# Kernel optimization log

Measured on AMD Instinct MI355X. Metric: run time of the kernel, lower is better.

The kernel has to match this reference:

```python
import jax, jax.numpy as jnp
import numpy as np

V, E, H = 1024, 32, 64
D = 8                     # number of tree levels (root at depth 0)
PER = 149796              # nodes per non-root level
N = 1 + 7 * PER           # 1048573 total nodes


def setup_inputs() -> dict:
    rng = np.random.default_rng(0)
    sizes = [1] + [PER] * (D - 1)
    off = np.concatenate([[0], np.cumsum(sizes)])
    depth = np.repeat(np.arange(D), sizes).astype(np.int64)
    parent = np.zeros(N, dtype=np.int64)  # root points to itself (harmless: its h is 0 when read)
    for l in range(1, D):
        parent[off[l]:off[l + 1]] = rng.integers(off[l - 1], off[l], sizes[l])
    token_ids = rng.integers(0, V, N).astype(np.int64)

    key = jax.random.key(0)
    ks = jax.random.split(key, 7)
    s = 0.05
    return {
        "token_ids": jnp.asarray(token_ids),
        "parent": jnp.asarray(parent),
        "depth": jnp.asarray(depth),
        "max_depth": D - 1,
        "emb": jax.random.normal(ks[0], (V, E), jnp.float32) * s,
        "W_iou_w": jax.random.normal(ks[1], (3 * H, E), jnp.float32) * s,
        "W_iou_b": jax.random.normal(ks[2], (3 * H,), jnp.float32) * s,
        "U_iou_w": jax.random.normal(ks[3], (3 * H, H), jnp.float32) * s,
        "W_f_w": jax.random.normal(ks[4], (H, E), jnp.float32) * s,
        "W_f_b": jax.random.normal(ks[5], (H,), jnp.float32) * s,
        "U_f_w": jax.random.normal(ks[6], (H, H), jnp.float32) * s,
    }


def reference(token_ids, parent, depth, max_depth, emb,
              W_iou_w, W_iou_b, U_iou_w, W_f_w, W_f_b, U_f_w):
    n = token_ids.shape[0]
    hid = U_f_w.shape[0]
    x = emb[token_ids]                                 # [N, E]
    wiou_x = x @ W_iou_w.T + W_iou_b                   # [N, 3H] (input part, precomputed)
    wf_x = x @ W_f_w.T + W_f_b                         # [N, H]
    h = jnp.zeros((n, hid), x.dtype)
    c = jnp.zeros((n, hid), x.dtype)
    # level-synchronous bottom-up sweep (deepest level first); children of a
    # depth-d node are exactly at depth d+1, already finalized when d is processed
    for d in range(max_depth, -1, -1):
        h_sum = jax.ops.segment_sum(h, parent, num_segments=n)        # child-sum per parent
        f = jax.nn.sigmoid(wf_x[parent] + h @ U_f_w.T)                # forget gate per child edge
        fc = jax.ops.segment_sum(f * c, parent, num_segments=n)      # sum_k f_k * c_k per parent
        iou = wiou_x + h_sum @ U_iou_w.T
        i, o, u = jnp.split(iou, 3, axis=-1)
        c_new = jax.nn.sigmoid(i) * jnp.tanh(u) + fc
        h_new = jax.nn.sigmoid(o) * jnp.tanh(c_new)
        m = (depth == d)[:, None]
        h = jnp.where(m, h_new, h)
        c = jnp.where(m, c_new, c)
    return h[0]  # root hidden state, matching TreeLSTMEncoder.forward
```

## Files before the change

### kernel.cpp

```cpp
#include <hip/hip_runtime.h>
#include <hip/hip_fp16.h>
#include <string.h>

#define PER  149796
#define NN   1048573
#define HDIM 64
#define EDIM 32
#define NIOU 192
#define NS   256

typedef _Float16 f16;
typedef _Float16 f16x8 __attribute__((ext_vector_type(8)));
typedef _Float16 f16x2 __attribute__((ext_vector_type(2)));
typedef float    f32x4 __attribute__((ext_vector_type(4)));

__device__ __forceinline__ float sigf(float x){ return 1.0f/(1.0f+__expf(-x)); }
__device__ __forceinline__ float tanh_f(float x){
  float ax = fabsf(x);
  float e  = __expf(-2.0f*ax);
  float t  = (1.0f - e)/(1.0f + e);
  return x < 0.0f ? -t : t;
}

__device__ __forceinline__ void atomAddH2(f16x2* p, f16 a, f16 b){
#if defined(__HIP_DEVICE_COMPILE__)
  typedef _Float16 h2 __attribute__((ext_vector_type(2)));
  h2 v; v[0]=a; v[1]=b;
  (void)__builtin_amdgcn_global_atomic_fadd_v2f16(
      (__attribute__((address_space(1))) h2*)p, v);
#else
  (void)p; (void)a; (void)b;
#endif
}

__global__ __launch_bounds__(256) void tablepack_kernel(
    const float* __restrict__ emb, const float* __restrict__ Wiou, const float* __restrict__ biou,
    const float* __restrict__ Wf, const float* __restrict__ bf,
    const float* __restrict__ Uf, const float* __restrict__ Uiou,
    float* __restrict__ embWiou, float* __restrict__ embWf,
    f16* __restrict__ Bfp, f16* __restrict__ Biop)
{
  if (blockIdx.x < 1024){
    int v = blockIdx.x;
    int m = threadIdx.x;
    const float* x = emb + (size_t)v*EDIM;
    if (m < NIOU){
      float a = biou[m];
      #pragma unroll
      for (int e=0;e<EDIM;e++) a += Wiou[m*EDIM+e]*x[e];
      embWiou[(size_t)v*NIOU + m] = a;
    } else {
      int mm = m - NIOU;
      float a = bf[mm];
      #pragma unroll
      for (int e=0;e<EDIM;e++) a += Wf[mm*EDIM+e]*x[e];
      embWf[(size_t)v*HDIM + mm] = a;
    }
  } else {
    for (int i = threadIdx.x; i < 2*4*64*8; i += 256){
      int j = i & 7, L = (i>>3)&63, st = i>>9;
      int t = st & 3, s = st >> 2;
      int k = s*32 + (L>>4)*8 + j;
      int n = t*16 + (L&15);
      Bfp[i] = (f16)Uf[n*HDIM + k];
    }
    for (int i = threadIdx.x; i < 2*12*64*8; i += 256){
      int j = i & 7, L = (i>>3)&63, st = i>>9;
      int t = st % 12, s = st / 12;
      int k = s*32 + (L>>4)*8 + j;
      int n = t*16 + (L&15);
      Biop[i] = (f16)Uiou[n*HDIM + k];
    }
  }
}

__global__ __launch_bounds__(64,4) void level_kernel(
    const int* __restrict__ tok, const int* __restrict__ parent,
    const float* __restrict__ embWiou, const float* __restrict__ embWf,
    const f16* __restrict__ Biopack, const f16* __restrict__ Ufpack,
    const f16x2* __restrict__ accIn, f16x2* __restrict__ accOut,
    float* __restrict__ rootslice,
    int poff, int ppoff, int mode)
{
  __shared__ f16 Ah[16*72];
  __shared__ f16 FAf[16*68];
  int lane = threadIdx.x;
  int j0   = blockIdx.x*16;
  int q = lane>>4, c16 = lane&15;

  const f16x8* Bp = (const f16x8*)Biopack;
  const f16x8* Up = (const f16x8*)Ufpack;

  f32x4 acc[12];
  #pragma unroll
  for (int nt=0;nt<12;nt++) acc[nt] = (f32x4){0.f,0.f,0.f,0.f};

  if (mode != 0){
    #pragma unroll
    for (int i=0;i<16;i++){
      int j = j0 + i; if (j > PER-1) j = PER-1;
      f16x2 v = accIn[(size_t)j*HDIM + lane];
      Ah[i*72 + lane]  = v.x;
      FAf[i*68 + lane] = v.y;
    }
    __syncthreads();
    f16x8 A0 = *(const f16x8*)(Ah + c16*72 + q*8);
    f16x8 A1 = *(const f16x8*)(Ah + c16*72 + 32 + q*8);
    #pragma unroll
    for (int nt=0;nt<12;nt++){
      f16x8 B0 = Bp[nt*64 + lane];
      f16x8 B1 = Bp[(12+nt)*64 + lane];
      acc[nt] = __builtin_amdgcn_mfma_f32_16x16x32_f16(A0, B0, acc[nt], 0,0,0);
      acc[nt] = __builtin_amdgcn_mfma_f32_16x16x32_f16(A1, B1, acc[nt], 0,0,0);
    }
  }

  int tok0 = (mode == 2) ? tok[0] : 0;
  float cc[4][4];
  f16   hh[4][4];
  int   prow_[4]; int wt_[4]; bool ok_[4];
  #pragma unroll
  for (int r=0;r<4;r++){
    int j = j0 + q*4 + r;
    bool ok = j < PER;
    int jl = ok ? j : PER-1;
    int g = poff + jl;
    int tk = tok[g];
    const float* tr = embWiou + (size_t)tk*NIOU;
    ok_[r] = ok;
    if (mode != 2){
      int pg = parent[g];
      prow_[r] = pg - ppoff;
      wt_[r]   = tok[pg];
    } else {
      prow_[r] = 0;
      wt_[r]   = tok0;
    }
    int lrow = q*4 + r;
    #pragma unroll
    for (int nt=0;nt<4;nt++){
      int col = nt*16 + c16;
      float ai = acc[nt][r]   + tr[col];
      float ao = acc[nt+4][r] + tr[64+col];
      float au = acc[nt+8][r] + tr[128+col];
      float fav = (mode != 0) ? (float)FAf[lrow*68 + col] : 0.0f;
      float c = sigf(ai)*tanh_f(au) + fav;
      float h = sigf(ao)*tanh_f(c);
      cc[r][nt] = c;
      hh[r][nt] = (f16)h;
    }
  }
  __syncthreads();
  #pragma unroll
  for (int r=0;r<4;r++)
    #pragma unroll
    for (int nt=0;nt<4;nt++)
      Ah[(q*4+r)*72 + nt*16 + c16] = hh[r][nt];
  __syncthreads();
  f16x8 H0 = *(const f16x8*)(Ah + c16*72 + q*8);
  f16x8 H1 = *(const f16x8*)(Ah + c16*72 + 32 + q*8);
  f32x4 g4[4];
  #pragma unroll
  for (int nt=0;nt<4;nt++) g4[nt] = (f32x4){0.f,0.f,0.f,0.f};
  #pragma unroll
  for (int nt=0;nt<4;nt++){
    f16x8 B0 = Up[nt*64 + lane];
    f16x8 B1 = Up[(4+nt)*64 + lane];
    g4[nt] = __builtin_amdgcn_mfma_f32_16x16x32_f16(H0, B0, g4[nt], 0,0,0);
    g4[nt] = __builtin_amdgcn_mfma_f32_16x16x32_f16(H1, B1, g4[nt], 0,0,0);
  }
  if (mode != 2){
    #pragma unroll
    for (int r=0;r<4;r++){
      if (!ok_[r]) continue;
      const float* wr = embWf + (size_t)wt_[r]*HDIM;
      size_t rb = (size_t)prow_[r]*HDIM;
      #pragma unroll
      for (int nt=0;nt<4;nt++){
        int col = nt*16 + c16;
        float v = sigf(g4[nt][r] + wr[col]) * cc[r][nt];
        atomAddH2(&accOut[rb + col], hh[r][nt], (f16)v);
      }
    }
  } else {
    const float* wr = embWf + (size_t)tok0*HDIM;
    float sH[4] = {0.f,0.f,0.f,0.f};
    float sF[4] = {0.f,0.f,0.f,0.f};
    #pragma unroll
    for (int r=0;r<4;r++){
      if (!ok_[r]) continue;
      #pragma unroll
      for (int nt=0;nt<4;nt++){
        int col = nt*16 + c16;
        float v = sigf(g4[nt][r] + wr[col]) * cc[r][nt];
        sH[nt] += (float)hh[r][nt];
        sF[nt] += v;
      }
    }
    int sl = blockIdx.x & (NS-1);
    #pragma unroll
    for (int nt=0;nt<4;nt++){
      int col = nt*16 + c16;
      atomicAdd(&rootslice[sl*128 + col],      sF[nt]);
      atomicAdd(&rootslice[sl*128 + 64 + col], sH[nt]);
    }
  }
}

__global__ void rootnode_kernel(
    const int* __restrict__ tok, const float* __restrict__ emb,
    const float* __restrict__ Wiou, const float* __restrict__ biou, const float* __restrict__ Uiou,
    const float* __restrict__ rootslice, float* __restrict__ out)
{
  __shared__ float hsh[64];
  int m = threadIdx.x;
  if (m >= HDIM) return;
  float fcs = 0.f, hs = 0.f;
  for (int s=0; s<NS; ++s){
    fcs += rootslice[s*128 + m];
    hs  += rootslice[s*128 + 64 + m];
  }
  hsh[m] = hs;
  __syncthreads();
  int t = tok[0];
  float ai=biou[m], ao=biou[HDIM+m], au=biou[2*HDIM+m];
  for (int e=0;e<EDIM;e++){
    float xe = emb[(size_t)t*EDIM+e];
    ai += Wiou[(size_t)m*EDIM+e]*xe;
    ao += Wiou[(size_t)(HDIM+m)*EDIM+e]*xe;
    au += Wiou[(size_t)(2*HDIM+m)*EDIM+e]*xe;
  }
  for (int k=0;k<HDIM;k++){
    float hv = hsh[k];
    ai += Uiou[(size_t)m*HDIM+k]*hv;
    ao += Uiou[(size_t)(HDIM+m)*HDIM+k]*hv;
    au += Uiou[(size_t)(2*HDIM+m)*HDIM+k]*hv;
  }
  float c = sigf(ai)*tanh_f(au) + fcs;
  out[m] = sigf(ao)*tanh_f(c);
}

static inline char* alignup(char* p){
  uintptr_t u = (uintptr_t)p;
  u = (u + 255) & ~(uintptr_t)255;
  return (char*)u;
}

extern "C" void kernel_launch(void* const* d_in, const int* in_sizes, int n_in,
                              void* d_out, int out_size, void* d_ws, size_t ws_size,
                              hipStream_t stream)
{
  const int*   tok    = (const int*)d_in[0];
  const int*   parent = (const int*)d_in[1];
  const float* emb    = (const float*)d_in[4];
  const float* Wiou   = (const float*)d_in[5];
  const float* biou   = (const float*)d_in[6];
  const float* Uiou   = (const float*)d_in[7];
  const float* Wf     = (const float*)d_in[8];
  const float* bf     = (const float*)d_in[9];
  const float* Uf     = (const float*)d_in[10];
  float* out = (float*)d_out;

  char* w = (char*)d_ws;
  size_t BUF = (size_t)PER*HDIM*sizeof(f16x2);
  f16x2* bufA      = (f16x2*)w;  w = alignup(w + BUF);
  f16x2* bufB      = (f16x2*)w;  w = alignup(w + BUF);
  float* embWiou   = (float*)w;  w = alignup(w + 1024*NIOU*sizeof(float));
  float* embWf     = (float*)w;  w = alignup(w + 1024*HDIM*sizeof(float));
  float* rootslice = (float*)w;  w = alignup(w + (size_t)NS*128*sizeof(float));
  f16*   Ufpack    = (f16*)w;    w = alignup(w + 2*4*64*8*sizeof(f16));
  f16*   Biopack   = (f16*)w;    w = alignup(w + 2*12*64*8*sizeof(f16));

  const int NB = (PER + 15)/16;

  (void)hipMemsetAsync(rootslice, 0, (size_t)NS*128*sizeof(float), stream);
  tablepack_kernel<<<1025, 256, 0, stream>>>(emb, Wiou, biou, Wf, bf, Uf, Uiou,
                                             embWiou, embWf, Ufpack, Biopack);

  (void)hipMemsetAsync(bufA, 0, BUF, stream);
  level_kernel<<<NB, 64, 0, stream>>>(tok, parent, embWiou, embWf, Biopack, Ufpack,
                                      bufB , bufA, rootslice,
                                      1 + 6*PER, 1 + 5*PER, 0);
  f16x2* accIn = bufA; f16x2* accOut = bufB;
  for (int d=6; d>=2; --d){
    (void)hipMemsetAsync(accOut, 0, BUF, stream);
    level_kernel<<<NB, 64, 0, stream>>>(tok, parent, embWiou, embWf, Biopack, Ufpack,
                                        accIn, accOut, rootslice,
                                        1 + (d-1)*PER, 1 + (d-2)*PER, 1);
    f16x2* t2 = accIn; accIn = accOut; accOut = t2;
  }
  level_kernel<<<NB, 64, 0, stream>>>(tok, parent, embWiou, embWf, Biopack, Ufpack,
                                      accIn, accOut , rootslice,
                                      1, 0, 2);

  rootnode_kernel<<<1, 64, 0, stream>>>(tok, emb, Wiou, biou, Uiou, rootslice, out);
}
```

Measured before the change: 593.5 us.

## Replace child-to-parent atomics with per-level sorted CSR segmented gather

```diff
diff --git a/kernel.cpp b/kernel.cpp
--- a/kernel.cpp
+++ b/kernel.cpp
@@ -1,18 +1,19 @@
 #include <hip/hip_runtime.h>
-#include <hip/hip_fp16.h>
-#include <string.h>
 
 #define PER  149796
-#define NN   1048573
 #define HDIM 64
 #define EDIM 32
 #define NIOU 192
+#define STG  96
 #define NS   256
 
 typedef _Float16 f16;
 typedef _Float16 f16x8 __attribute__((ext_vector_type(8)));
 typedef _Float16 f16x2 __attribute__((ext_vector_type(2)));
 typedef float    f32x4 __attribute__((ext_vector_type(4)));
+
+typedef __attribute__((address_space(1))) const unsigned gu32;
+typedef __attribute__((address_space(3))) unsigned lu32;
 
 __device__ __forceinline__ float sigf(float x){ return 1.0f/(1.0f+__expf(-x)); }
 __device__ __forceinline__ float tanh_f(float x){
@@ -22,15 +23,90 @@
   return x < 0.0f ? -t : t;
 }
 
-__device__ __forceinline__ void atomAddH2(f16x2* p, f16 a, f16 b){
-#if defined(__HIP_DEVICE_COMPILE__)
-  typedef _Float16 h2 __attribute__((ext_vector_type(2)));
-  h2 v; v[0]=a; v[1]=b;
-  (void)__builtin_amdgcn_global_atomic_fadd_v2f16(
-      (__attribute__((address_space(1))) h2*)p, v);
-#else
-  (void)p; (void)a; (void)b;
-#endif
+
+__global__ __launch_bounds__(256) void init1_kernel(
+    const int* __restrict__ tok, int* __restrict__ spos,
+    int* __restrict__ stok1, int* __restrict__ ptok1, int* __restrict__ soff_all)
+{
+  int i = blockIdx.x*256 + threadIdx.x;
+  if (i < PER){
+    spos[i]  = i;
+    stok1[i] = tok[1+i];
+    ptok1[i] = tok[0];
+  }
+  if (i < 6) soff_all[(size_t)i*(PER+1) + PER] = PER;
+}
+
+__global__ __launch_bounds__(256) void countL_kernel(
+    const int* __restrict__ parent, const int* __restrict__ spos_cur,
+    int* __restrict__ cnt, int coff, int poff)
+{
+  int i = blockIdx.x*256 + threadIdx.x;
+  if (i >= PER) return;
+  int s = spos_cur[parent[coff+i] - poff];
+  atomicAdd(&cnt[s], 1);
+}
+
+__global__ __launch_bounds__(256) void scan1_kernel(const int* __restrict__ cnt, int* __restrict__ bsum){
+  __shared__ int sc[256];
+  int b=blockIdx.x, t=threadIdx.x;
+  int base=b*1024+t*4;
+  int s=0;
+  #pragma unroll
+  for (int e=0;e<4;e++){ int idx=base+e; if (idx<PER) s+=cnt[idx]; }
+  sc[t]=s; __syncthreads();
+  for (int d=128; d>0; d>>=1){ if (t<d) sc[t]+=sc[t+d]; __syncthreads(); }
+  if (t==0) bsum[b]=sc[0];
+}
+
+__global__ __launch_bounds__(256) void scan23_kernel(
+    const int* __restrict__ cnt, const int* __restrict__ bsum,
+    int* __restrict__ soff, int* __restrict__ cursor)
+{
+  __shared__ int bb[256];
+  __shared__ int sc[256];
+  int b=blockIdx.x, t=threadIdx.x;
+  const int nb = (PER + 1023)/1024;
+  bb[t] = (t<nb)? bsum[t] : 0;
+  __syncthreads();
+  for (int d=1; d<256; d<<=1){
+    int v=(t>=d)?bb[t-d]:0; __syncthreads();
+    bb[t]+=v; __syncthreads();
+  }
+  int bbase = (b==0)?0:bb[b-1];
+  int base=b*1024+t*4;
+  int e0=(base  <PER)?cnt[base  ]:0;
+  int e1=(base+1<PER)?cnt[base+1]:0;
+  int e2=(base+2<PER)?cnt[base+2]:0;
+  int e3=(base+3<PER)?cnt[base+3]:0;
+  sc[t]=e0+e1+e2+e3; __syncthreads();
+  for (int d=1; d<256; d<<=1){
+    int v=(t>=d)?sc[t-d]:0; __syncthreads();
+    sc[t]+=v; __syncthreads();
+  }
+  int x = bbase + ((t==0)?0:sc[t-1]);
+  if (base  <PER){ soff[base  ]=x;          cursor[base  ]=x; }
+  if (base+1<PER){ soff[base+1]=x+e0;       cursor[base+1]=x+e0; }
+  if (base+2<PER){ soff[base+2]=x+e0+e1;    cursor[base+2]=x+e0+e1; }
+  if (base+3<PER){ soff[base+3]=x+e0+e1+e2; cursor[base+3]=x+e0+e1+e2; }
+}
+
+__global__ __launch_bounds__(256) void scatterL_kernel(
+    const int* __restrict__ parent, const int* __restrict__ tok,
+    const int* __restrict__ spos_cur, int* __restrict__ cursor,
+    int* __restrict__ spos_next, int* __restrict__ stok_next, int* __restrict__ ptok_next,
+    int* __restrict__ cnt, int coff, int poff)
+{
+  int i = blockIdx.x*256 + threadIdx.x;
+  if (i >= PER) return;
+  cnt[i] = 0;
+  int g  = coff + i;
+  int pg = parent[g];
+  int s  = spos_cur[pg - poff];
+  int pos = atomicAdd(&cursor[s], 1);
+  spos_next[i]   = pos;
+  stok_next[pos] = tok[g];
+  ptok_next[pos] = tok[pg];
 }
 
 __global__ __launch_bounds__(256) void tablepack_kernel(
@@ -74,38 +150,73 @@
   }
 }
 
-__global__ __launch_bounds__(64,4) void level_kernel(
-    const int* __restrict__ tok, const int* __restrict__ parent,
+__global__ __launch_bounds__(256) void level_kernel(
+    const int* __restrict__ stokL, const int* __restrict__ ptokL,
+    const int* __restrict__ soffL,
     const float* __restrict__ embWiou, const float* __restrict__ embWf,
     const f16* __restrict__ Biopack, const f16* __restrict__ Ufpack,
-    const f16x2* __restrict__ accIn, f16x2* __restrict__ accOut,
-    float* __restrict__ rootslice,
-    int poff, int ppoff, int mode)
-{
-  __shared__ f16 Ah[16*72];
-  __shared__ f16 FAf[16*68];
-  int lane = threadIdx.x;
-  int j0   = blockIdx.x*16;
+    const f16x2* __restrict__ HFin, f16x2* __restrict__ HFout,
+    float* __restrict__ rootslice, int mode)
+{
+  __shared__ __align__(16) char smem[STG*HDIM*4];
+  f16x2* stage = (f16x2*)smem;
+  f16*   Ah    = (f16*)smem;
+  f16*   FAf   = (f16*)(smem + 9216);
+  int lane = threadIdx.x & 63;
+  int wv   = __builtin_amdgcn_readfirstlane(threadIdx.x >> 6);
+  int p0   = wv*16;
+  int j0b  = blockIdx.x*64;
+  int j0   = j0b + p0;
   int q = lane>>4, c16 = lane&15;
 
+  float hs[16], fa[16];
+  #pragma unroll
+  for (int i=0;i<16;i++){ hs[i]=0.f; fa[i]=0.f; }
+
+  if (mode != 0){
+    int ei = j0b + 64; if (ei > PER) ei = PER;
+    int S = soffL[j0b];
+    int E = soffL[ei];
+    int sB[17];
+    #pragma unroll
+    for (int i=0;i<=16;i++){
+      int jj = j0 + i; if (jj > PER) jj = PER;
+      sB[i] = soffL[jj];
+    }
+    const unsigned* HFinU = (const unsigned*)HFin;
+    for (int cb = S; cb < E; cb += STG){
+      int n = E - cb; if (n > STG) n = STG;
+      for (int r = wv; r < n; r += 4){
+        gu32* gp = (gu32*)(HFinU + (size_t)(cb+r)*HDIM) + lane;
+        __builtin_amdgcn_global_load_lds(gp, (lu32*)&stage[r*HDIM], 4, 0, 0);
+      }
+      __syncthreads();
+      int lim = cb + n;
+      #pragma unroll
+      for (int i=0;i<16;i++){
+        int lo = sB[i]   > cb  ? sB[i]   : cb;
+        int hi = sB[i+1] < lim ? sB[i+1] : lim;
+        for (int p=lo; p<hi; ++p){
+          f16x2 v = stage[(p-cb)*HDIM + lane];
+          hs[i] += (float)v.x; fa[i] += (float)v.y;
+        }
+      }
+      __syncthreads();
+    }
+  }
+  #pragma unroll
+  for (int i=0;i<16;i++){
+    Ah[(p0+i)*72 + lane]  = (f16)hs[i];
+    FAf[(p0+i)*68 + lane] = (f16)fa[i];
+  }
+  __syncthreads();
   const f16x8* Bp = (const f16x8*)Biopack;
-  const f16x8* Up = (const f16x8*)Ufpack;
-
   f32x4 acc[12];
   #pragma unroll
   for (int nt=0;nt<12;nt++) acc[nt] = (f32x4){0.f,0.f,0.f,0.f};
-
   if (mode != 0){
-    #pragma unroll
-    for (int i=0;i<16;i++){
-      int j = j0 + i; if (j > PER-1) j = PER-1;
-      f16x2 v = accIn[(size_t)j*HDIM + lane];
-      Ah[i*72 + lane]  = v.x;
-      FAf[i*68 + lane] = v.y;
-    }
-    __syncthreads();
-    f16x8 A0 = *(const f16x8*)(Ah + c16*72 + q*8);
-    f16x8 A1 = *(const f16x8*)(Ah + c16*72 + 32 + q*8);
+    f16x8 A0 = *(const f16x8*)(Ah + (p0+c16)*72 + q*8);
+    f16x8 A1 = *(const f16x8*)(Ah + (p0+c16)*72 + 32 + q*8);
     #pragma unroll
     for (int nt=0;nt<12;nt++){
       f16x8 B0 = Bp[nt*64 + lane];
@@ -114,36 +225,26 @@
       acc[nt] = __builtin_amdgcn_mfma_f32_16x16x32_f16(A1, B1, acc[nt], 0,0,0);
     }
   }
-
-  int tok0 = (mode == 2) ? tok[0] : 0;
   float cc[4][4];
   f16   hh[4][4];
-  int   prow_[4]; int wt_[4]; bool ok_[4];
+  int   wt_[4]; bool ok_[4];
   #pragma unroll
   for (int r=0;r<4;r++){
     int j = j0 + q*4 + r;
     bool ok = j < PER;
     int jl = ok ? j : PER-1;
-    int g = poff + jl;
-    int tk = tok[g];
+    int tk = stokL[jl];
     const float* tr = embWiou + (size_t)tk*NIOU;
+    wt_[r] = ptokL[jl];
     ok_[r] = ok;
-    if (mode != 2){
-      int pg = parent[g];
-      prow_[r] = pg - ppoff;
-      wt_[r]   = tok[pg];
-    } else {
-      prow_[r] = 0;
-      wt_[r]   = tok0;
-    }
-    int lrow = q*4 + r;
+    int lrow = p0 + q*4 + r;
     #pragma unroll
     for (int nt=0;nt<4;nt++){
       int col = nt*16 + c16;
       float ai = acc[nt][r]   + tr[col];
       float ao = acc[nt+4][r] + tr[64+col];
       float au = acc[nt+8][r] + tr[128+col];
-      float fav = (mode != 0) ? (float)FAf[lrow*68 + col] : 0.0f;
+      float fav = (float)FAf[lrow*68 + col];
       float c = sigf(ai)*tanh_f(au) + fav;
       float h = sigf(ao)*tanh_f(c);
       cc[r][nt] = c;
@@ -155,10 +256,11 @@
   for (int r=0;r<4;r++)
     #pragma unroll
     for (int nt=0;nt<4;nt++)
-      Ah[(q*4+r)*72 + nt*16 + c16] = hh[r][nt];
+      Ah[(p0+q*4+r)*72 + nt*16 + c16] = hh[r][nt];
   __syncthreads();
-  f16x8 H0 = *(const f16x8*)(Ah + c16*72 + q*8);
-  f16x8 H1 = *(const f16x8*)(Ah + c16*72 + 32 + q*8);
+  f16x8 H0 = *(const f16x8*)(Ah + (p0+c16)*72 + q*8);
+  f16x8 H1 = *(const f16x8*)(Ah + (p0+c16)*72 + 32 + q*8);
+  const f16x8* Up = (const f16x8*)Ufpack;
   f32x4 g4[4];
   #pragma unroll
   for (int nt=0;nt<4;nt++) g4[nt] = (f32x4){0.f,0.f,0.f,0.f};
@@ -174,21 +276,22 @@
     for (int r=0;r<4;r++){
       if (!ok_[r]) continue;
       const float* wr = embWf + (size_t)wt_[r]*HDIM;
-      size_t rb = (size_t)prow_[r]*HDIM;
+      int j = j0 + q*4 + r;
       #pragma unroll
       for (int nt=0;nt<4;nt++){
         int col = nt*16 + c16;
         float v = sigf(g4[nt][r] + wr[col]) * cc[r][nt];
-        atomAddH2(&accOut[rb + col], hh[r][nt], (f16)v);
+        f16x2 o; o.x = hh[r][nt]; o.y = (f16)v;
+        HFout[(size_t)j*HDIM + col] = o;
       }
     }
   } else {
-    const float* wr = embWf + (size_t)tok0*HDIM;
     float sH[4] = {0.f,0.f,0.f,0.f};
     float sF[4] = {0.f,0.f,0.f,0.f};
     #pragma unroll
     for (int r=0;r<4;r++){
       if (!ok_[r]) continue;
+      const float* wr = embWf + (size_t)wt_[r]*HDIM;
       #pragma unroll
       for (int nt=0;nt<4;nt++){
         int col = nt*16 + c16;
@@ -197,7 +300,7 @@
         sF[nt] += v;
       }
     }
-    int sl = blockIdx.x & (NS-1);
+    int sl = (blockIdx.x*4 + wv) & (NS-1);
     #pragma unroll
     for (int nt=0;nt<4;nt++){
       int col = nt*16 + c16;
@@ -263,35 +366,62 @@
 
   char* w = (char*)d_ws;
   size_t BUF = (size_t)PER*HDIM*sizeof(f16x2);
-  f16x2* bufA      = (f16x2*)w;  w = alignup(w + BUF);
-  f16x2* bufB      = (f16x2*)w;  w = alignup(w + BUF);
+  f16x2* HFA       = (f16x2*)w;  w = alignup(w + BUF);
+  f16x2* HFB       = (f16x2*)w;  w = alignup(w + BUF);
+  int*   sposA     = (int*)w;    w = alignup(w + (size_t)PER*sizeof(int));
+  int*   sposB     = (int*)w;    w = alignup(w + (size_t)PER*sizeof(int));
+  int*   cnt       = (int*)w;    w = alignup(w + (size_t)PER*sizeof(int));
+  int*   cursor    = (int*)w;    w = alignup(w + (size_t)PER*sizeof(int));
+  int*   bsum      = (int*)w;    w = alignup(w + 256*sizeof(int));
+  int*   soff_all  = (int*)w;    w = alignup(w + (size_t)6*(PER+1)*sizeof(int));
+  int*   stok_all  = (int*)w;    w = alignup(w + (size_t)7*PER*sizeof(int));
+  int*   ptok_all  = (int*)w;    w = alignup(w + (size_t)7*PER*sizeof(int));
   float* embWiou   = (float*)w;  w = alignup(w + 1024*NIOU*sizeof(float));
   float* embWf     = (float*)w;  w = alignup(w + 1024*HDIM*sizeof(float));
   float* rootslice = (float*)w;  w = alignup(w + (size_t)NS*128*sizeof(float));
   f16*   Ufpack    = (f16*)w;    w = alignup(w + 2*4*64*8*sizeof(f16));
   f16*   Biopack   = (f16*)w;    w = alignup(w + 2*12*64*8*sizeof(f16));
 
-  const int NB = (PER + 15)/16;
-
+  const int gPER = (PER + 255)/256;
+  const int gSCN = (PER + 1023)/1024;
+  const int NBL  = (PER + 63)/64;
+
+  (void)hipMemsetAsync(cnt, 0, (size_t)PER*sizeof(int), stream);
   (void)hipMemsetAsync(rootslice, 0, (size_t)NS*128*sizeof(float), stream);
   tablepack_kernel<<<1025, 256, 0, stream>>>(emb, Wiou, biou, Wf, bf, Uf, Uiou,
                                              embWiou, embWf, Ufpack, Biopack);
-
-  (void)hipMemsetAsync(bufA, 0, BUF, stream);
-  level_kernel<<<NB, 64, 0, stream>>>(tok, parent, embWiou, embWf, Biopack, Ufpack,
-                                      bufB , bufA, rootslice,
-                                      1 + 6*PER, 1 + 5*PER, 0);
-  f16x2* accIn = bufA; f16x2* accOut = bufB;
+  init1_kernel<<<gPER, 256, 0, stream>>>(tok, sposA, stok_all, ptok_all, soff_all);
+
+  int* spos_cur = sposA; int* spos_nxt = sposB;
+  for (int d=1; d<=6; ++d){
+    int poff = 1 + (d-1)*PER;
+    int coff = 1 + d*PER;
+    countL_kernel <<<gPER, 256, 0, stream>>>(parent, spos_cur, cnt, coff, poff);
+    scan1_kernel  <<<gSCN, 256, 0, stream>>>(cnt, bsum);
+    scan23_kernel <<<gSCN, 256, 0, stream>>>(cnt, bsum,
+                                             soff_all + (size_t)(d-1)*(PER+1), cursor);
+    scatterL_kernel<<<gPER, 256, 0, stream>>>(parent, tok, spos_cur, cursor, spos_nxt,
+                                              stok_all + (size_t)d*PER,
+                                              ptok_all + (size_t)d*PER,
+                                              cnt, coff, poff);
+    int* t2 = spos_cur; spos_cur = spos_nxt; spos_nxt = t2;
+  }
+
+  level_kernel<<<NBL, 256, 0, stream>>>(stok_all + (size_t)6*PER, ptok_all + (size_t)6*PER,
+                                        nullptr, embWiou, embWf, Biopack, Ufpack,
+                                        nullptr, HFA, rootslice, 0);
+  f16x2* in = HFA; f16x2* ob = HFB;
   for (int d=6; d>=2; --d){
-    (void)hipMemsetAsync(accOut, 0, BUF, stream);
-    level_kernel<<<NB, 64, 0, stream>>>(tok, parent, embWiou, embWf, Biopack, Ufpack,
-                                        accIn, accOut, rootslice,
-                                        1 + (d-1)*PER, 1 + (d-2)*PER, 1);
-    f16x2* t2 = accIn; accIn = accOut; accOut = t2;
-  }
-  level_kernel<<<NB, 64, 0, stream>>>(tok, parent, embWiou, embWf, Biopack, Ufpack,
-                                      accIn, accOut , rootslice,
-                                      1, 0, 2);
+    level_kernel<<<NBL, 256, 0, stream>>>(stok_all + (size_t)(d-1)*PER,
+                                          ptok_all + (size_t)(d-1)*PER,
+                                          soff_all + (size_t)(d-1)*(PER+1),
+                                          embWiou, embWf, Biopack, Ufpack,
+                                          in, ob, rootslice, 1);
+    f16x2* t2 = in; in = ob; ob = t2;
+  }
+  level_kernel<<<NBL, 256, 0, stream>>>(stok_all, ptok_all, soff_all,
+                                        embWiou, embWf, Biopack, Ufpack,
+                                        in, ob , rootslice, 2);
 
   rootnode_kernel<<<1, 64, 0, stream>>>(tok, emb, Wiou, biou, Uiou, rootslice, out);
 }
```

Measured after the change: 655.4 us. 1.1x slower.
